# Kernel optimization log

Measured on AMD Instinct MI355X. Metric: run time of the kernel, lower is better.

## Reference

```python
import jax, jax.numpy as jnp
import numpy as np

EMBED_DIM = 1024
NUM_HEADS = 16
HEAD_DIM = EMBED_DIM // NUM_HEADS
BATCH, SEQ = 1, 4096


def setup_inputs() -> dict:
    key = jax.random.key(0)
    ks = jax.random.split(key, 9)
    s = 1.0 / np.sqrt(EMBED_DIM)
    x = jax.random.normal(ks[0], (BATCH, SEQ, EMBED_DIM), dtype=jnp.float32)
    def lin(kw, kb):
        W = jax.random.uniform(kw, (EMBED_DIM, EMBED_DIM), jnp.float32, -s, s)
        b = jax.random.uniform(kb, (EMBED_DIM,), jnp.float32, -s, s)
        return W, b
    Wq, bq = lin(ks[1], ks[2])
    Wk, bk = lin(ks[3], ks[4])
    Wv, bv = lin(ks[5], ks[6])
    Wo, bo = lin(ks[7], ks[8])
    return {"x": x, "Wq": Wq, "bq": bq, "Wk": Wk, "bk": bk,
            "Wv": Wv, "bv": bv, "Wo": Wo, "bo": bo}


def _split_heads(t):  # [B,S,E] -> [B,H,S,D]
    B, S, _ = t.shape
    return t.reshape(B, S, NUM_HEADS, HEAD_DIM).transpose(0, 2, 1, 3)


def reference(x, Wq, bq, Wk, bk, Wv, bv, Wo, bo):
    scale = HEAD_DIM ** -0.5
    q = _split_heads(x @ Wq.T + bq)
    k = _split_heads(x @ Wk.T + bk)
    v = _split_heads(x @ Wv.T + bv)
    # explicit attention matrix, as in the torch module
    scores = jnp.einsum('bhqd,bhkd->bhqk', q * scale, k)
    weights = jax.nn.softmax(scores, axis=-1)
    out = jnp.einsum('bhqk,bhkd->bhqd', weights, v)
    B, H, S, D = out.shape
    out = out.transpose(0, 2, 1, 3).reshape(B, S, H * D)
    return out @ Wo.T + bo
```

## Files before the change

### kernel.cpp

```cpp
#include <hip/hip_runtime.h>


typedef unsigned short u16;
using bf16x8 = __attribute__((ext_vector_type(8))) __bf16;
using bf16x4 = __attribute__((ext_vector_type(4))) __bf16;
using f32x4  = __attribute__((ext_vector_type(4))) float;

__device__ __forceinline__ u16 f2bf(float f) {
  unsigned u = __float_as_uint(f);
  u += 0x7fffu + ((u >> 16) & 1u);
  return (u16)(u >> 16);
}
__device__ __forceinline__ float bf2f(u16 h) {
  return __uint_as_float(((unsigned)h) << 16);
}
__device__ __forceinline__ float fexp2(float x) {
  return __builtin_amdgcn_exp2f(x);
}

#define GLOAD16(gptr, lptr)                                                   \
  __builtin_amdgcn_global_load_lds(                                           \
      (const __attribute__((address_space(1))) unsigned int*)(gptr),          \
      (__attribute__((address_space(3))) unsigned int*)(lptr), 16, 0, 0)

__device__ __forceinline__ f32x4 mfma16(bf16x8 a, bf16x8 b, f32x4 c) {
  return __builtin_amdgcn_mfma_f32_16x16x32_bf16(a, b, c, 0, 0, 0);
}

__device__ __forceinline__ bf16x8 lds_read8(const u16* base, int row, int col) {
  int boff = (row * 128 + col * 2) ^ ((row & 7) << 4);
  return *(const bf16x8*)((const char*)base + boff);
}

__global__ void cvt_all(const float* __restrict__ x, const float* __restrict__ Wq,
                        const float* __restrict__ Wk, const float* __restrict__ Wv,
                        const float* __restrict__ Wo, u16* __restrict__ xb,
                        u16* __restrict__ Wqb, u16* __restrict__ Wkb,
                        u16* __restrict__ Wvb, u16* __restrict__ Woh,
                        u16* __restrict__ Wol) {
  int b = blockIdx.x;
  if (b < 7168) {
    const float* src; u16* dst; int base;
    if (b < 4096)      { src = x;  dst = xb;  base = b; }
    else if (b < 5120) { src = Wq; dst = Wqb; base = b - 4096; }
    else if (b < 6144) { src = Wk; dst = Wkb; base = b - 5120; }
    else               { src = Wv; dst = Wvb; base = b - 6144; }
    int i = base * 256 + threadIdx.x;
    float4 v = ((const float4*)src)[i];
    ushort4 o;
    o.x = f2bf(v.x); o.y = f2bf(v.y); o.z = f2bf(v.z); o.w = f2bf(v.w);
    ((ushort4*)dst)[i] = o;
  } else {
    int i = (b - 7168) * 256 + threadIdx.x;
    float4 v = ((const float4*)Wo)[i];
    ushort4 h, l;
    h.x = f2bf(v.x); l.x = f2bf(v.x - bf2f(h.x));
    h.y = f2bf(v.y); l.y = f2bf(v.y - bf2f(h.y));
    h.z = f2bf(v.z); l.z = f2bf(v.z - bf2f(h.z));
    h.w = f2bf(v.w); l.w = f2bf(v.w - bf2f(h.w));
    ((ushort4*)Woh)[i] = h;
    ((ushort4*)Wol)[i] = l;
  }
}

struct GemmMat {
  const u16* Bh;
  const float* bias;
  u16* oh;
  u16* ovt;
  float scale;
};
struct GemmParams {
  const u16* Ah;
  GemmMat mm[3];
};

__global__ __launch_bounds__(256, 2) void gemm_qkv(GemmParams p) {
  const int tid = threadIdx.x;
  const int lane = tid & 63, w = tid >> 6;
  const int wr = w >> 1, wc = w & 1;
  const int lg = lane >> 4, lr = lane & 15;
  const GemmMat g = p.mm[blockIdx.z];
  const int brow = blockIdx.y, bcol = blockIdx.x;

  __shared__ u16 As[128 * 32];
  __shared__ u16 Bs[128 * 32];

  f32x4 acc[4][4];
#pragma unroll
  for (int m = 0; m < 4; ++m)
#pragma unroll
    for (int n = 0; n < 4; ++n) acc[m][n] = f32x4{0.f, 0.f, 0.f, 0.f};

  for (int k0 = 0; k0 < 1024; k0 += 32) {
#pragma unroll
    for (int it = 0; it < 2; ++it) {
      int c = tid + it * 256;
      int row = c >> 2, cc = c & 3;
      size_t ga = (size_t)(brow * 128 + row) * 1024 + k0 + cc * 8;
      size_t gb = (size_t)(bcol * 128 + row) * 1024 + k0 + cc * 8;
      GLOAD16(p.Ah + ga, &As[c * 8]);
      GLOAD16(g.Bh + gb, &Bs[c * 8]);
    }
    __syncthreads();

    bf16x8 a[4], b[4];
#pragma unroll
    for (int m = 0; m < 4; ++m)
      a[m] = *(const bf16x8*)&As[(64 * wr + 16 * m + lr) * 32 + 8 * lg];
#pragma unroll
    for (int n = 0; n < 4; ++n)
      b[n] = *(const bf16x8*)&Bs[(64 * wc + 16 * n + lr) * 32 + 8 * lg];
#pragma unroll
    for (int m = 0; m < 4; ++m)
#pragma unroll
      for (int n = 0; n < 4; ++n) acc[m][n] = mfma16(a[m], b[n], acc[m][n]);
    __syncthreads();
  }

#pragma unroll
  for (int n = 0; n < 4; ++n) {
    int gcol = bcol * 128 + 64 * wc + 16 * n + lr;
    float bs = g.bias[gcol];
#pragma unroll
    for (int m = 0; m < 4; ++m) {
      int grow0 = brow * 128 + 64 * wr + 16 * m + 4 * lg;
      float v0 = (acc[m][n][0] + bs) * g.scale;
      float v1 = (acc[m][n][1] + bs) * g.scale;
      float v2 = (acc[m][n][2] + bs) * g.scale;
      float v3 = (acc[m][n][3] + bs) * g.scale;
      if (g.ovt) {
        ushort4 hs;
        hs.x = f2bf(v0); hs.y = f2bf(v1); hs.z = f2bf(v2); hs.w = f2bf(v3);
        *(ushort4*)&g.ovt[(size_t)gcol * 4096 + grow0] = hs;
      } else {
        g.oh[(size_t)(grow0 + 0) * 1024 + gcol] = f2bf(v0);
        g.oh[(size_t)(grow0 + 1) * 1024 + gcol] = f2bf(v1);
        g.oh[(size_t)(grow0 + 2) * 1024 + gcol] = f2bf(v2);
        g.oh[(size_t)(grow0 + 3) * 1024 + gcol] = f2bf(v3);
      }
    }
  }
}

__global__ __launch_bounds__(256, 2) void gemm_out64(
    const u16* __restrict__ Ah, const u16* __restrict__ Al,
    const u16* __restrict__ Bh, const u16* __restrict__ Bl,
    const float* __restrict__ bias, float* __restrict__ out) {
  const int tid = threadIdx.x;
  const int lane = tid & 63, w = tid >> 6;
  const int lg = lane >> 4, lr = lane & 15;
  const int brow = blockIdx.y, bcol = blockIdx.x;

  __shared__ u16 As[2][64 * 32];
  __shared__ u16 Bs[2][128 * 32];

  f32x4 acc[4][2];
#pragma unroll
  for (int m = 0; m < 4; ++m)
#pragma unroll
    for (int n = 0; n < 2; ++n) acc[m][n] = f32x4{0.f, 0.f, 0.f, 0.f};

  for (int k0 = 0; k0 < 1024; k0 += 32) {
    {
      int c = tid;
      int row = c >> 2, cc = c & 3;
      size_t ga = (size_t)(brow * 64 + row) * 1024 + k0 + cc * 8;
      GLOAD16(Ah + ga, &As[0][c * 8]);
      GLOAD16(Al + ga, &As[1][c * 8]);
    }
#pragma unroll
    for (int it = 0; it < 2; ++it) {
      int c = tid + it * 256;
      int row = c >> 2, cc = c & 3;
      size_t gb = (size_t)(bcol * 128 + row) * 1024 + k0 + cc * 8;
      GLOAD16(Bh + gb, &Bs[0][c * 8]);
      GLOAD16(Bl + gb, &Bs[1][c * 8]);
    }
    __syncthreads();

    bf16x8 a[4], a2[4], b[2], b2[2];
#pragma unroll
    for (int m = 0; m < 4; ++m) {
      int off = (16 * m + lr) * 32 + 8 * lg;
      a[m]  = *(const bf16x8*)&As[0][off];
      a2[m] = *(const bf16x8*)&As[1][off];
    }
#pragma unroll
    for (int n = 0; n < 2; ++n) {
      int off = (32 * w + 16 * n + lr) * 32 + 8 * lg;
      b[n]  = *(const bf16x8*)&Bs[0][off];
      b2[n] = *(const bf16x8*)&Bs[1][off];
    }
#pragma unroll
    for (int m = 0; m < 4; ++m)
#pragma unroll
      for (int n = 0; n < 2; ++n) {
        acc[m][n] = mfma16(a[m], b[n], acc[m][n]);
        acc[m][n] = mfma16(a[m], b2[n], acc[m][n]);
        acc[m][n] = mfma16(a2[m], b[n], acc[m][n]);
      }
    __syncthreads();
  }

#pragma unroll
  for (int n = 0; n < 2; ++n) {
    int gcol = bcol * 128 + 32 * w + 16 * n + lr;
    float bs = bias[gcol];
#pragma unroll
    for (int m = 0; m < 4; ++m) {
      int grow0 = brow * 64 + 16 * m + 4 * lg;
#pragma unroll
      for (int j = 0; j < 4; ++j)
        out[(size_t)(grow0 + j) * 1024 + gcol] = acc[m][n][j] + bs;
    }
  }
}

__global__ __launch_bounds__(256, 2) void attn_kernel(
    const u16* __restrict__ Qb, const u16* __restrict__ Kb,
    const u16* __restrict__ Vt, u16* __restrict__ ctxh,
    u16* __restrict__ ctxl) {
  const int tid = threadIdx.x;
  const int lane = tid & 63, w = tid >> 6;
  const int lg = lane >> 4, lr = lane & 15;
  const int h = blockIdx.x;
  const int q0 = blockIdx.y * 128;

  __shared__ u16 Ks[2][64 * 64];
  __shared__ u16 Vs[2][64 * 64];
  __shared__ u16 Ps[4][2][16 * 64];

  bf16x8 qf[2][2];
#pragma unroll
  for (int qs = 0; qs < 2; ++qs) {
    size_t qbase = (size_t)(q0 + 32 * w + 16 * qs + lr) * 1024 + h * 64;
    qf[qs][0] = *(const bf16x8*)&Qb[qbase + 8 * lg];
    qf[qs][1] = *(const bf16x8*)&Qb[qbase + 32 + 8 * lg];
  }

  bf16x8 ones;
#pragma unroll
  for (int i = 0; i < 8; ++i) ones[i] = (__bf16)1.0f;

  f32x4 o[2][4], lacc[2];
#pragma unroll
  for (int qs = 0; qs < 2; ++qs) {
    lacc[qs] = f32x4{0.f, 0.f, 0.f, 0.f};
#pragma unroll
    for (int n = 0; n < 4; ++n) o[qs][n] = f32x4{0.f, 0.f, 0.f, 0.f};
  }

  auto stage = [&](int buf, int kv0) {
#pragma unroll
    for (int it = 0; it < 2; ++it) {
      int c = tid + it * 256;
      int row = c >> 3, cc = c & 7;
      int scc = cc ^ (row & 7);
      GLOAD16(Kb + (size_t)(kv0 + row) * 1024 + h * 64 + scc * 8,
              &Ks[buf][c * 8]);
      GLOAD16(Vt + (size_t)(h * 64 + row) * 4096 + kv0 + scc * 8,
              &Vs[buf][c * 8]);
    }
  };

  stage(0, 0);

  for (int t = 0; t < 64; ++t) {
    const int cur = t & 1;
    if (t < 63) {
      stage(cur ^ 1, (t + 1) * 64);
      asm volatile("s_waitcnt vmcnt(4)" ::: "memory");
    } else {
      asm volatile("s_waitcnt vmcnt(0)" ::: "memory");
    }
    __builtin_amdgcn_s_barrier();

    f32x4 s[2][4];
#pragma unroll
    for (int qs = 0; qs < 2; ++qs)
#pragma unroll
      for (int nb = 0; nb < 4; ++nb) s[qs][nb] = f32x4{0.f, 0.f, 0.f, 0.f};
    __builtin_amdgcn_s_setprio(1);
#pragma unroll
    for (int nb = 0; nb < 4; ++nb)
#pragma unroll
      for (int ks = 0; ks < 2; ++ks) {
        bf16x8 kf = lds_read8(&Ks[cur][0], 16 * nb + lr, 32 * ks + 8 * lg);
        s[0][nb] = mfma16(kf, qf[0][ks], s[0][nb]);
        s[1][nb] = mfma16(kf, qf[1][ks], s[1][nb]);
      }
    __builtin_amdgcn_s_setprio(0);

#pragma unroll
    for (int qs = 0; qs < 2; ++qs)
#pragma unroll
      for (int nb = 0; nb < 4; ++nb) {
        bf16x4 pk;
        pk[0] = (__bf16)fexp2(s[qs][nb][0]);
        pk[1] = (__bf16)fexp2(s[qs][nb][1]);
        pk[2] = (__bf16)fexp2(s[qs][nb][2]);
        pk[3] = (__bf16)fexp2(s[qs][nb][3]);
        int boff = (lr * 128 + (16 * nb + 4 * lg) * 2) ^ ((lr & 7) << 4);
        *(bf16x4*)((char*)&Ps[w][qs][0] + boff) = pk;
      }

    __builtin_amdgcn_s_setprio(1);
#pragma unroll
    for (int ks = 0; ks < 2; ++ks) {
      bf16x8 pf0 = lds_read8(&Ps[w][0][0], lr, 32 * ks + 8 * lg);
      bf16x8 pf1 = lds_read8(&Ps[w][1][0], lr, 32 * ks + 8 * lg);
      lacc[0] = mfma16(ones, pf0, lacc[0]);
      lacc[1] = mfma16(ones, pf1, lacc[1]);
#pragma unroll
      for (int nb = 0; nb < 4; ++nb) {
        bf16x8 vf = lds_read8(&Vs[cur][0], 16 * nb + lr, 32 * ks + 8 * lg);
        o[0][nb] = mfma16(vf, pf0, o[0][nb]);
        o[1][nb] = mfma16(vf, pf1, o[1][nb]);
      }
    }
    __builtin_amdgcn_s_setprio(0);

    __builtin_amdgcn_s_barrier();
  }

#pragma unroll
  for (int qs = 0; qs < 2; ++qs) {
    const float linv = 1.0f / lacc[qs][0];
    const size_t grow = (size_t)(q0 + 32 * w + 16 * qs + lr) * 1024;
#pragma unroll
    for (int nb = 0; nb < 4; ++nb) {
      ushort4 hs, ls;
      float v0 = o[qs][nb][0] * linv, v1 = o[qs][nb][1] * linv;
      float v2 = o[qs][nb][2] * linv, v3 = o[qs][nb][3] * linv;
      hs.x = f2bf(v0); ls.x = f2bf(v0 - bf2f(hs.x));
      hs.y = f2bf(v1); ls.y = f2bf(v1 - bf2f(hs.y));
      hs.z = f2bf(v2); ls.z = f2bf(v2 - bf2f(hs.z));
      hs.w = f2bf(v3); ls.w = f2bf(v3 - bf2f(hs.w));
      size_t gc = grow + h * 64 + 16 * nb + 4 * lg;
      *(ushort4*)&ctxh[gc] = hs;
      *(ushort4*)&ctxl[gc] = ls;
    }
  }
}

extern "C" void kernel_launch(void* const* d_in, const int* in_sizes, int n_in,
                              void* d_out, int out_size, void* d_ws,
                              size_t ws_size, hipStream_t stream) {
  const float* x  = (const float*)d_in[0];
  const float* Wq = (const float*)d_in[1];
  const float* bq = (const float*)d_in[2];
  const float* Wk = (const float*)d_in[3];
  const float* bk = (const float*)d_in[4];
  const float* Wv = (const float*)d_in[5];
  const float* bv = (const float*)d_in[6];
  const float* Wo = (const float*)d_in[7];
  const float* bo = (const float*)d_in[8];

  const size_t M1 = 1024u * 1024u;
  u16* p = (u16*)d_ws;
  u16* xb   = p + 0;
  u16* Qb   = p + 4 * M1;
  u16* Kb   = p + 8 * M1;
  u16* ctxl = p + 12 * M1;
  u16* Vtb  = p + 16 * M1;
  u16* Wqb  = p + 20 * M1;
  u16* Wkb  = p + 21 * M1;
  u16* Wvb  = p + 22 * M1;
  u16* Woh  = p + 23 * M1;
  u16* Wol  = p + 24 * M1;
  u16* ctxh = xb;

  cvt_all<<<8192, 256, 0, stream>>>(x, Wq, Wk, Wv, Wo, xb, Wqb, Wkb, Wvb, Woh,
                                    Wol);

  GemmParams pq;
  pq.Ah = xb;
  pq.mm[0] = {Wqb, bq, Qb, nullptr, 0.125f * 1.44269504f};
  pq.mm[1] = {Wkb, bk, Kb, nullptr, 1.0f};
  pq.mm[2] = {Wvb, bv, nullptr, Vtb, 1.0f};
  gemm_qkv<<<dim3(8, 32, 3), 256, 0, stream>>>(pq);

  attn_kernel<<<dim3(16, 32), 256, 0, stream>>>(Qb, Kb, Vtb, ctxh, ctxl);

  gemm_out64<<<dim3(8, 64), 256, 0, stream>>>(ctxh, ctxl, Woh, Wol, bo,
                                              (float*)d_out);
}
```

Measured before the change: 167.9 us.

## Use two waves of 64 query rows each in attention, splitting KV tile in halves

The attention block drops from four waves of 32 query rows to two waves of 64 rows each, so every K and V fragment read from LDS feeds four MFMAs instead of two. Each 64-key tile is processed in two 32-key halves, which keeps the score registers and the per-wave P buffer small. The row sum is now accumulated in scalar registers and reduced with shuffles at the end, replacing the extra MFMA against a ones vector. In exchange each block has half as many waves, so latency hiding and occupancy drop, and register pressure rises from the larger O accumulator.

```diff
diff --git a/kernel.cpp b/kernel.cpp
--- a/kernel.cpp
+++ b/kernel.cpp
@@ -217,49 +217,57 @@
   }
 }
 
-__global__ __launch_bounds__(256, 2) void attn_kernel(
+__global__ __launch_bounds__(128, 2) void attn_kernel(
     const u16* __restrict__ Qb, const u16* __restrict__ Kb,
     const u16* __restrict__ Vt, u16* __restrict__ ctxh,
     u16* __restrict__ ctxl) {
   const int tid = threadIdx.x;
   const int lane = tid & 63, w = tid >> 6;
   const int lg = lane >> 4, lr = lane & 15;
-  const int h = blockIdx.x;
+  const int hd = blockIdx.x;
   const int q0 = blockIdx.y * 128;
 
   __shared__ u16 Ks[2][64 * 64];
   __shared__ u16 Vs[2][64 * 64];
-  __shared__ u16 Ps[4][2][16 * 64];
-
-  bf16x8 qf[2][2];
-#pragma unroll
-  for (int qs = 0; qs < 2; ++qs) {
-    size_t qbase = (size_t)(q0 + 32 * w + 16 * qs + lr) * 1024 + h * 64;
+  __shared__ u16 Ps[2][64 * 32];
+
+  bf16x8 qf[4][2];
+#pragma unroll
+  for (int qs = 0; qs < 4; ++qs) {
+    size_t qbase = (size_t)(q0 + 64 * w + 16 * qs + lr) * 1024 + hd * 64;
     qf[qs][0] = *(const bf16x8*)&Qb[qbase + 8 * lg];
     qf[qs][1] = *(const bf16x8*)&Qb[qbase + 32 + 8 * lg];
   }
 
-  bf16x8 ones;
-#pragma unroll
-  for (int i = 0; i < 8; ++i) ones[i] = (__bf16)1.0f;
-
-  f32x4 o[2][4], lacc[2];
-#pragma unroll
-  for (int qs = 0; qs < 2; ++qs) {
-    lacc[qs] = f32x4{0.f, 0.f, 0.f, 0.f};
+  f32x4 o[4][4];
+  float lsum[4];
+#pragma unroll
+  for (int qs = 0; qs < 4; ++qs) {
+    lsum[qs] = 0.f;
 #pragma unroll
     for (int n = 0; n < 4; ++n) o[qs][n] = f32x4{0.f, 0.f, 0.f, 0.f};
   }
 
+  char* const pbase = (char*)&Ps[w][0];
+  auto poff = [&](int q, int kvi) {
+    return ((q * 64 + kvi * 2)) ^ ((q & 3) << 4);
+  };
+
   auto stage = [&](int buf, int kv0) {
 #pragma unroll
-    for (int it = 0; it < 2; ++it) {
-      int c = tid + it * 256;
-      int row = c >> 3, cc = c & 7;
-      int scc = cc ^ (row & 7);
-      GLOAD16(Kb + (size_t)(kv0 + row) * 1024 + h * 64 + scc * 8,
+    for (int it = 0; it < 4; ++it) {
+      int c = tid + it * 128;
+      int kv = c >> 3, cc = c & 7;
+      int scc = cc ^ (kv & 7);
+      GLOAD16(Kb + (size_t)(kv0 + kv) * 1024 + hd * 64 + scc * 8,
               &Ks[buf][c * 8]);
-      GLOAD16(Vt + (size_t)(h * 64 + row) * 4096 + kv0 + scc * 8,
+    }
+#pragma unroll
+    for (int it = 0; it < 4; ++it) {
+      int c = tid + it * 128;
+      int d = c >> 3, cc = c & 7;
+      int scc = cc ^ (d & 7);
+      GLOAD16(Vt + (size_t)(hd * 64 + d) * 4096 + kv0 + scc * 8,
               &Vs[buf][c * 8]);
     }
   };
@@ -270,74 +278,87 @@
     const int cur = t & 1;
     if (t < 63) {
       stage(cur ^ 1, (t + 1) * 64);
-      asm volatile("s_waitcnt vmcnt(4)" ::: "memory");
+      asm volatile("s_waitcnt vmcnt(8)" ::: "memory");
     } else {
       asm volatile("s_waitcnt vmcnt(0)" ::: "memory");
     }
     __builtin_amdgcn_s_barrier();
 
-    f32x4 s[2][4];
-#pragma unroll
-    for (int qs = 0; qs < 2; ++qs)
-#pragma unroll
-      for (int nb = 0; nb < 4; ++nb) s[qs][nb] = f32x4{0.f, 0.f, 0.f, 0.f};
-    __builtin_amdgcn_s_setprio(1);
-#pragma unroll
-    for (int nb = 0; nb < 4; ++nb)
-#pragma unroll
-      for (int ks = 0; ks < 2; ++ks) {
-        bf16x8 kf = lds_read8(&Ks[cur][0], 16 * nb + lr, 32 * ks + 8 * lg);
-        s[0][nb] = mfma16(kf, qf[0][ks], s[0][nb]);
-        s[1][nb] = mfma16(kf, qf[1][ks], s[1][nb]);
+#pragma unroll
+    for (int wb = 0; wb < 2; ++wb) {
+      f32x4 s[4][2];
+#pragma unroll
+      for (int qs = 0; qs < 4; ++qs)
+#pragma unroll
+        for (int h = 0; h < 2; ++h) s[qs][h] = f32x4{0.f, 0.f, 0.f, 0.f};
+      __builtin_amdgcn_s_setprio(1);
+#pragma unroll
+      for (int h = 0; h < 2; ++h)
+#pragma unroll
+        for (int ks = 0; ks < 2; ++ks) {
+          bf16x8 kf =
+              lds_read8(&Ks[cur][0], 32 * wb + 16 * h + lr, 32 * ks + 8 * lg);
+          s[0][h] = mfma16(kf, qf[0][ks], s[0][h]);
+          s[1][h] = mfma16(kf, qf[1][ks], s[1][h]);
+          s[2][h] = mfma16(kf, qf[2][ks], s[2][h]);
+          s[3][h] = mfma16(kf, qf[3][ks], s[3][h]);
+        }
+      __builtin_amdgcn_s_setprio(0);
+
+#pragma unroll
+      for (int qs = 0; qs < 4; ++qs)
+#pragma unroll
+        for (int h = 0; h < 2; ++h) {
+          float e0 = fexp2(s[qs][h][0]);
+          float e1 = fexp2(s[qs][h][1]);
+          float e2 = fexp2(s[qs][h][2]);
+          float e3 = fexp2(s[qs][h][3]);
+          lsum[qs] += (e0 + e1) + (e2 + e3);
+          bf16x4 pk;
+          pk[0] = (__bf16)e0; pk[1] = (__bf16)e1;
+          pk[2] = (__bf16)e2; pk[3] = (__bf16)e3;
+          *(bf16x4*)(pbase + poff(16 * qs + lr, 16 * h + 4 * lg)) = pk;
+        }
+
+      __builtin_amdgcn_s_setprio(1);
+      bf16x8 pf[4];
+#pragma unroll
+      for (int qs = 0; qs < 4; ++qs)
+        pf[qs] = *(const bf16x8*)(pbase + poff(16 * qs + lr, 8 * lg));
+#pragma unroll
+      for (int nbd = 0; nbd < 4; ++nbd) {
+        bf16x8 vf = lds_read8(&Vs[cur][0], 16 * nbd + lr, 32 * wb + 8 * lg);
+        o[0][nbd] = mfma16(vf, pf[0], o[0][nbd]);
+        o[1][nbd] = mfma16(vf, pf[1], o[1][nbd]);
+        o[2][nbd] = mfma16(vf, pf[2], o[2][nbd]);
+        o[3][nbd] = mfma16(vf, pf[3], o[3][nbd]);
       }
-    __builtin_amdgcn_s_setprio(0);
-
-#pragma unroll
-    for (int qs = 0; qs < 2; ++qs)
-#pragma unroll
-      for (int nb = 0; nb < 4; ++nb) {
-        bf16x4 pk;
-        pk[0] = (__bf16)fexp2(s[qs][nb][0]);
-        pk[1] = (__bf16)fexp2(s[qs][nb][1]);
-        pk[2] = (__bf16)fexp2(s[qs][nb][2]);
-        pk[3] = (__bf16)fexp2(s[qs][nb][3]);
-        int boff = (lr * 128 + (16 * nb + 4 * lg) * 2) ^ ((lr & 7) << 4);
-        *(bf16x4*)((char*)&Ps[w][qs][0] + boff) = pk;
-      }
-
-    __builtin_amdgcn_s_setprio(1);
-#pragma unroll
-    for (int ks = 0; ks < 2; ++ks) {
-      bf16x8 pf0 = lds_read8(&Ps[w][0][0], lr, 32 * ks + 8 * lg);
-      bf16x8 pf1 = lds_read8(&Ps[w][1][0], lr, 32 * ks + 8 * lg);
-      lacc[0] = mfma16(ones, pf0, lacc[0]);
-      lacc[1] = mfma16(ones, pf1, lacc[1]);
-#pragma unroll
-      for (int nb = 0; nb < 4; ++nb) {
-        bf16x8 vf = lds_read8(&Vs[cur][0], 16 * nb + lr, 32 * ks + 8 * lg);
-        o[0][nb] = mfma16(vf, pf0, o[0][nb]);
-        o[1][nb] = mfma16(vf, pf1, o[1][nb]);
-      }
-    }
-    __builtin_amdgcn_s_setprio(0);
+      __builtin_amdgcn_s_setprio(0);
+    }
 
     __builtin_amdgcn_s_barrier();
   }
 
 #pragma unroll
-  for (int qs = 0; qs < 2; ++qs) {
-    const float linv = 1.0f / lacc[qs][0];
-    const size_t grow = (size_t)(q0 + 32 * w + 16 * qs + lr) * 1024;
-#pragma unroll
-    for (int nb = 0; nb < 4; ++nb) {
+  for (int qs = 0; qs < 4; ++qs) {
+    lsum[qs] += __shfl_xor(lsum[qs], 16);
+    lsum[qs] += __shfl_xor(lsum[qs], 32);
+  }
+
+#pragma unroll
+  for (int qs = 0; qs < 4; ++qs) {
+    const float linv = 1.0f / lsum[qs];
+    const size_t grow = (size_t)(q0 + 64 * w + 16 * qs + lr) * 1024;
+#pragma unroll
+    for (int nbd = 0; nbd < 4; ++nbd) {
       ushort4 hs, ls;
-      float v0 = o[qs][nb][0] * linv, v1 = o[qs][nb][1] * linv;
-      float v2 = o[qs][nb][2] * linv, v3 = o[qs][nb][3] * linv;
+      float v0 = o[qs][nbd][0] * linv, v1 = o[qs][nbd][1] * linv;
+      float v2 = o[qs][nbd][2] * linv, v3 = o[qs][nbd][3] * linv;
       hs.x = f2bf(v0); ls.x = f2bf(v0 - bf2f(hs.x));
       hs.y = f2bf(v1); ls.y = f2bf(v1 - bf2f(hs.y));
       hs.z = f2bf(v2); ls.z = f2bf(v2 - bf2f(hs.z));
       hs.w = f2bf(v3); ls.w = f2bf(v3 - bf2f(hs.w));
-      size_t gc = grow + h * 64 + 16 * nb + 4 * lg;
+      size_t gc = grow + hd * 64 + 16 * nbd + 4 * lg;
       *(ushort4*)&ctxh[gc] = hs;
       *(ushort4*)&ctxl[gc] = ls;
     }
@@ -381,7 +402,7 @@
   pq.mm[2] = {Wvb, bv, nullptr, Vtb, 1.0f};
   gemm_qkv<<<dim3(8, 32, 3), 256, 0, stream>>>(pq);
 
-  attn_kernel<<<dim3(16, 32), 256, 0, stream>>>(Qb, Kb, Vtb, ctxh, ctxl);
+  attn_kernel<<<dim3(16, 32), 128, 0, stream>>>(Qb, Kb, Vtb, ctxh, ctxl);
 
   gemm_out64<<<dim3(8, 64), 256, 0, stream>>>(ctxh, ctxl, Woh, Wol, bo,
                                               (float*)d_out);
```

New measurement: 217.3 us. 29.4% more time.

## Software-pipeline attention PV with next QK, and widen QKV GEMM K-tile to 64

Applied to the files above, without the earlier changes.

The attention loop now runs the P·V product of the previous tile after the QK^T of the current tile, so exp/softmax work overlaps with MFMA work. It uses a triple-buffered V tile and double-buffered P, and drops one barrier per iteration. The QKV GEMM stages 64-wide K tiles with an XOR swizzle, which halves the number of barrier rounds and reduces LDS bank conflicts. In exchange the kernels use more LDS, which may lower occupancy, and the buffer-rotation logic is more complex.

```diff
diff --git a/kernel.cpp b/kernel.cpp
--- a/kernel.cpp
+++ b/kernel.cpp
@@ -83,8 +83,8 @@
   const GemmMat g = p.mm[blockIdx.z];
   const int brow = blockIdx.y, bcol = blockIdx.x;
 
-  __shared__ u16 As[128 * 32];
-  __shared__ u16 Bs[128 * 32];
+  __shared__ u16 As[128 * 64];
+  __shared__ u16 Bs[128 * 64];
 
   f32x4 acc[4][4];
 #pragma unroll
@@ -92,29 +92,37 @@
 #pragma unroll
     for (int n = 0; n < 4; ++n) acc[m][n] = f32x4{0.f, 0.f, 0.f, 0.f};
 
-  for (int k0 = 0; k0 < 1024; k0 += 32) {
-#pragma unroll
-    for (int it = 0; it < 2; ++it) {
+  for (int k0 = 0; k0 < 1024; k0 += 64) {
+#pragma unroll
+    for (int it = 0; it < 4; ++it) {
       int c = tid + it * 256;
-      int row = c >> 2, cc = c & 3;
-      size_t ga = (size_t)(brow * 128 + row) * 1024 + k0 + cc * 8;
-      size_t gb = (size_t)(bcol * 128 + row) * 1024 + k0 + cc * 8;
+      int row = c >> 3, cc = c & 7;
+      int scc = cc ^ (row & 7);
+      size_t ga = (size_t)(brow * 128 + row) * 1024 + k0 + scc * 8;
+      size_t gb = (size_t)(bcol * 128 + row) * 1024 + k0 + scc * 8;
       GLOAD16(p.Ah + ga, &As[c * 8]);
       GLOAD16(g.Bh + gb, &Bs[c * 8]);
     }
     __syncthreads();
 
-    bf16x8 a[4], b[4];
+    bf16x8 a[4][2], b[4][2];
 #pragma unroll
     for (int m = 0; m < 4; ++m)
-      a[m] = *(const bf16x8*)&As[(64 * wr + 16 * m + lr) * 32 + 8 * lg];
+#pragma unroll
+      for (int kk = 0; kk < 2; ++kk)
+        a[m][kk] = lds_read8(As, 64 * wr + 16 * m + lr, 32 * kk + 8 * lg);
 #pragma unroll
     for (int n = 0; n < 4; ++n)
-      b[n] = *(const bf16x8*)&Bs[(64 * wc + 16 * n + lr) * 32 + 8 * lg];
+#pragma unroll
+      for (int kk = 0; kk < 2; ++kk)
+        b[n][kk] = lds_read8(Bs, 64 * wc + 16 * n + lr, 32 * kk + 8 * lg);
 #pragma unroll
     for (int m = 0; m < 4; ++m)
 #pragma unroll
-      for (int n = 0; n < 4; ++n) acc[m][n] = mfma16(a[m], b[n], acc[m][n]);
+      for (int n = 0; n < 4; ++n) {
+        acc[m][n] = mfma16(a[m][0], b[n][0], acc[m][n]);
+        acc[m][n] = mfma16(a[m][1], b[n][1], acc[m][n]);
+      }
     __syncthreads();
   }
 
@@ -224,17 +232,17 @@
   const int tid = threadIdx.x;
   const int lane = tid & 63, w = tid >> 6;
   const int lg = lane >> 4, lr = lane & 15;
-  const int h = blockIdx.x;
+  const int hd = blockIdx.x;
   const int q0 = blockIdx.y * 128;
 
   __shared__ u16 Ks[2][64 * 64];
-  __shared__ u16 Vs[2][64 * 64];
-  __shared__ u16 Ps[4][2][16 * 64];
+  __shared__ u16 Vs[3][64 * 64];
+  __shared__ u16 Ps[4][2][2][16 * 64];
 
   bf16x8 qf[2][2];
 #pragma unroll
   for (int qs = 0; qs < 2; ++qs) {
-    size_t qbase = (size_t)(q0 + 32 * w + 16 * qs + lr) * 1024 + h * 64;
+    size_t qbase = (size_t)(q0 + 32 * w + 16 * qs + lr) * 1024 + hd * 64;
     qf[qs][0] = *(const bf16x8*)&Qb[qbase + 8 * lg];
     qf[qs][1] = *(const bf16x8*)&Qb[qbase + 32 + 8 * lg];
   }
@@ -251,29 +259,59 @@
     for (int n = 0; n < 4; ++n) o[qs][n] = f32x4{0.f, 0.f, 0.f, 0.f};
   }
 
-  auto stage = [&](int buf, int kv0) {
+  auto stageK = [&](int buf, int kv0) {
 #pragma unroll
     for (int it = 0; it < 2; ++it) {
       int c = tid + it * 256;
-      int row = c >> 3, cc = c & 7;
-      int scc = cc ^ (row & 7);
-      GLOAD16(Kb + (size_t)(kv0 + row) * 1024 + h * 64 + scc * 8,
+      int kv = c >> 3, cc = c & 7;
+      int scc = cc ^ (kv & 7);
+      GLOAD16(Kb + (size_t)(kv0 + kv) * 1024 + hd * 64 + scc * 8,
               &Ks[buf][c * 8]);
-      GLOAD16(Vt + (size_t)(h * 64 + row) * 4096 + kv0 + scc * 8,
+    }
+  };
+  auto stageV = [&](int buf, int kv0) {
+#pragma unroll
+    for (int it = 0; it < 2; ++it) {
+      int c = tid + it * 256;
+      int d = c >> 3, cc = c & 7;
+      int scc = cc ^ (d & 7);
+      GLOAD16(Vt + (size_t)(hd * 64 + d) * 4096 + kv0 + scc * 8,
               &Vs[buf][c * 8]);
     }
   };
 
-  stage(0, 0);
+  auto pv = [&](int vbuf, int ph) {
+    __builtin_amdgcn_s_setprio(1);
+#pragma unroll
+    for (int ks = 0; ks < 2; ++ks) {
+      bf16x8 pf0 = lds_read8(&Ps[w][ph][0][0], lr, 32 * ks + 8 * lg);
+      bf16x8 pf1 = lds_read8(&Ps[w][ph][1][0], lr, 32 * ks + 8 * lg);
+      lacc[0] = mfma16(ones, pf0, lacc[0]);
+      lacc[1] = mfma16(ones, pf1, lacc[1]);
+#pragma unroll
+      for (int nb = 0; nb < 4; ++nb) {
+        bf16x8 vf = lds_read8(&Vs[vbuf][0], 16 * nb + lr, 32 * ks + 8 * lg);
+        o[0][nb] = mfma16(vf, pf0, o[0][nb]);
+        o[1][nb] = mfma16(vf, pf1, o[1][nb]);
+      }
+    }
+    __builtin_amdgcn_s_setprio(0);
+  };
+
+  stageK(0, 0);
+  stageV(0, 0);
+
+  int vprev = 2, vcur = 0, vnext = 1;
 
   for (int t = 0; t < 64; ++t) {
-    const int cur = t & 1;
     if (t < 63) {
-      stage(cur ^ 1, (t + 1) * 64);
+      stageK((t + 1) & 1, (t + 1) * 64);
+      stageV(vnext, (t + 1) * 64);
       asm volatile("s_waitcnt vmcnt(4)" ::: "memory");
     } else {
       asm volatile("s_waitcnt vmcnt(0)" ::: "memory");
     }
+    asm volatile("s_waitcnt lgkmcnt(0)" ::: "memory");
     __builtin_amdgcn_s_barrier();
 
     f32x4 s[2][4];
@@ -281,16 +319,19 @@
     for (int qs = 0; qs < 2; ++qs)
 #pragma unroll
       for (int nb = 0; nb < 4; ++nb) s[qs][nb] = f32x4{0.f, 0.f, 0.f, 0.f};
+    const u16* kbase = &Ks[t & 1][0];
     __builtin_amdgcn_s_setprio(1);
 #pragma unroll
     for (int nb = 0; nb < 4; ++nb)
 #pragma unroll
       for (int ks = 0; ks < 2; ++ks) {
-        bf16x8 kf = lds_read8(&Ks[cur][0], 16 * nb + lr, 32 * ks + 8 * lg);
+        bf16x8 kf = lds_read8(kbase, 16 * nb + lr, 32 * ks + 8 * lg);
         s[0][nb] = mfma16(kf, qf[0][ks], s[0][nb]);
         s[1][nb] = mfma16(kf, qf[1][ks], s[1][nb]);
       }
     __builtin_amdgcn_s_setprio(0);
+
+    if (t > 0) pv(vprev, (t - 1) & 1);
 
 #pragma unroll
     for (int qs = 0; qs < 2; ++qs)
@@ -302,27 +343,13 @@
         pk[2] = (__bf16)fexp2(s[qs][nb][2]);
         pk[3] = (__bf16)fexp2(s[qs][nb][3]);
         int boff = (lr * 128 + (16 * nb + 4 * lg) * 2) ^ ((lr & 7) << 4);
-        *(bf16x4*)((char*)&Ps[w][qs][0] + boff) = pk;
-      }
-
-    __builtin_amdgcn_s_setprio(1);
-#pragma unroll
-    for (int ks = 0; ks < 2; ++ks) {
-      bf16x8 pf0 = lds_read8(&Ps[w][0][0], lr, 32 * ks + 8 * lg);
-      bf16x8 pf1 = lds_read8(&Ps[w][1][0], lr, 32 * ks + 8 * lg);
-      lacc[0] = mfma16(ones, pf0, lacc[0]);
-      lacc[1] = mfma16(ones, pf1, lacc[1]);
-#pragma unroll
-      for (int nb = 0; nb < 4; ++nb) {
-        bf16x8 vf = lds_read8(&Vs[cur][0], 16 * nb + lr, 32 * ks + 8 * lg);
-        o[0][nb] = mfma16(vf, pf0, o[0][nb]);
-        o[1][nb] = mfma16(vf, pf1, o[1][nb]);
-      }
-    }
-    __builtin_amdgcn_s_setprio(0);
-
-    __builtin_amdgcn_s_barrier();
-  }
+        *(bf16x4*)((char*)&Ps[w][t & 1][qs][0] + boff) = pk;
+      }
+
+    int tmp = vprev; vprev = vcur; vcur = vnext; vnext = tmp;
+  }
+
+  pv(vprev, 1);
 
 #pragma unroll
   for (int qs = 0; qs < 2; ++qs) {
@@ -337,7 +364,7 @@
       hs.y = f2bf(v1); ls.y = f2bf(v1 - bf2f(hs.y));
       hs.z = f2bf(v2); ls.z = f2bf(v2 - bf2f(hs.z));
       hs.w = f2bf(v3); ls.w = f2bf(v3 - bf2f(hs.w));
-      size_t gc = grow + h * 64 + 16 * nb + 4 * lg;
+      size_t gc = grow + hd * 64 + 16 * nb + 4 * lg;
       *(ushort4*)&ctxh[gc] = hs;
       *(ushort4*)&ctxl[gc] = ls;
     }
```

Result: faster. 163.5 us (-2.6%).
